# Optimization experiments

Measured on AMD Instinct MI355X. Metric: run time of the kernel, lower is better.

The kernel has to match this reference:

```python
import jax, jax.numpy as jnp
import numpy as np

T, D, N = 131072, 512, 8


def setup_inputs() -> dict:
    key = jax.random.key(0)
    k1, k2, k3, k4 = jax.random.split(key, 4)
    x = jax.random.normal(k1, (T, D), dtype=jnp.float32)
    branch_idx = jax.random.randint(k2, (T,), 0, N, dtype=jnp.int32)
    # module inits weight to identity and bias to zero; use random values
    # (scaled like a trained projection) for a meaningful correctness test
    weight = jax.random.normal(k3, (N, D, D), dtype=jnp.float32) * (1.0 / np.sqrt(D))
    bias = jax.random.normal(k4, (N, D), dtype=jnp.float32) * 0.02
    return {"x": x, "branch_idx": branch_idx, "weight": weight, "bias": bias}


def reference(x, branch_idx, weight, bias):
    # Math: out[t] = x[t] @ weight[branch_idx[t]] + bias[branch_idx[t]]
    # Instead of materializing the gathered (T, D, D) weight tensor (as the
    # naive torch code does), run one dense GEMM per branch and select the
    # rows belonging to that branch. Same result, far less HBM traffic.
    num_branches = weight.shape[0]
    out = jnp.take(bias, branch_idx, axis=0)  # (T, D) gathered bias
    for n in range(num_branches):  # small fixed loop over branches
        mask = (branch_idx == n)[:, None]  # (T, 1)
        out = out + jnp.where(mask, x @ weight[n], jnp.zeros((), x.dtype))
    return out
```

## Files before the change

### kernel.cpp

```cpp
#include <hip/hip_runtime.h>
#include <hip/hip_bf16.h>
#include <stdint.h>

#define T_TOK 131072
#define DIM   512
#define NBR   8
#define BM    64
#define BK    32
#define NKT   (DIM / BK)
#define GT    512
#define MT    288

typedef __attribute__((ext_vector_type(8))) __bf16 bf16x8;
typedef __attribute__((ext_vector_type(4))) float  f32x4;

__device__ __forceinline__ unsigned short f2bf(float f) {
  union { float f; unsigned int u; } v; v.f = f;
  unsigned int r = v.u + 0x7fffu + ((v.u >> 16) & 1u);
  return (unsigned short)(r >> 16);
}


__global__ void k_init(int* counts) {
  if (threadIdx.x < NBR) counts[threadIdx.x] = 0;
}

__global__ __launch_bounds__(512) void k_bhist(const int* __restrict__ bidx,
                                               int* __restrict__ counts) {
  __shared__ int h[NBR];
  if (threadIdx.x < NBR) h[threadIdx.x] = 0;
  __syncthreads();
  int t = blockIdx.x * 512 + threadIdx.x;
  atomicAdd(&h[bidx[t]], 1);
  __syncthreads();
  if (threadIdx.x < NBR) atomicAdd(&counts[threadIdx.x], h[threadIdx.x]);
}

__global__ void k_off(const int* __restrict__ counts, int* __restrict__ offsets,
                      int* __restrict__ cursors) {
  if (threadIdx.x == 0) {
    int s = 0;
    for (int n = 0; n < NBR; ++n) { offsets[n] = s; cursors[n] = s; s += counts[n]; }
  }
}

__global__ __launch_bounds__(512) void k_scatter(const int* __restrict__ bidx,
                                                 int* __restrict__ cursors,
                                                 int* __restrict__ perm) {
  __shared__ int h[NBR], base[NBR];
  if (threadIdx.x < NBR) h[threadIdx.x] = 0;
  __syncthreads();
  int t = blockIdx.x * 512 + threadIdx.x;
  int b = bidx[t];
  int rank = atomicAdd(&h[b], 1);
  __syncthreads();
  if (threadIdx.x < NBR)
    base[threadIdx.x] = atomicAdd(&cursors[threadIdx.x], h[threadIdx.x]);
  __syncthreads();
  perm[base[b] + rank] = t;
}

__global__ __launch_bounds__(256) void k_wtrans(const float* __restrict__ W,
                                                unsigned short* __restrict__ Wt) {
  __shared__ float tile[BK][129];
  int blk = blockIdx.x;
  int b  = blk >> 6;
  int kt = (blk >> 2) & 15;
  int cb = blk & 3;
  int t = threadIdx.x;
  #pragma unroll
  for (int i = 0; i < 4; ++i) {
    int idx4 = i * 256 + t;
    int kr = idx4 >> 5;
    int c4 = idx4 & 31;
    const float* src = W + (((size_t)b * DIM + (size_t)(kt * BK + kr)) * DIM + cb * 128 + c4 * 4);
    float4 v = *(const float4*)src;
    tile[kr][c4 * 4 + 0] = v.x;
    tile[kr][c4 * 4 + 1] = v.y;
    tile[kr][c4 * 4 + 2] = v.z;
    tile[kr][c4 * 4 + 3] = v.w;
  }
  __syncthreads();
  int c  = t >> 1;
  int kh = t & 1;
  unsigned int p[8];
  #pragma unroll
  for (int i = 0; i < 8; ++i) {
    unsigned short lo = f2bf(tile[kh * 16 + i * 2 + 0][c]);
    unsigned short hi = f2bf(tile[kh * 16 + i * 2 + 1][c]);
    p[i] = (unsigned int)lo | ((unsigned int)hi << 16);
  }
  size_t obase = (((size_t)b * 16 + kt) * DIM + (size_t)(cb * 128 + c)) * BK + kh * 16;
  uint4 q0; q0.x = p[0]; q0.y = p[1]; q0.z = p[2]; q0.w = p[3];
  uint4 q1; q1.x = p[4]; q1.y = p[5]; q1.z = p[6]; q1.w = p[7];
  *(uint4*)&Wt[obase]     = q0;
  *(uint4*)&Wt[obase + 8] = q1;
}

__global__ __launch_bounds__(GT, 4)
void k_gemm(const float* __restrict__ x, const float* __restrict__ bias,
            const unsigned short* __restrict__ Wt,
            const int* __restrict__ counts, const int* __restrict__ offsets,
            const int* __restrict__ perm, float* __restrict__ out) {
  __shared__ __align__(16) unsigned short As[2][BM * 40];
  __shared__ int rowIdx[BM];

  const int tid = threadIdx.x;
  const int l = tid & 63;
  const int w = tid >> 6;

  const int b  = blockIdx.x / MT;
  const int lt = blockIdx.x % MT;
  const int cnt = counts[b];
  const int row0 = lt * BM;
  if (row0 >= cnt) return;
  const int gstart = offsets[b];
  const int vrows = min(BM, cnt - row0);

  if (tid < BM) {
    int r = row0 + tid; if (r >= cnt) r = cnt - 1;
    rowIdx[tid] = perm[gstart + r];
  }
  __syncthreads();

  const int arow = tid >> 3;
  const int kq = tid & 7;
  const float* aptr = x + (size_t)rowIdx[arow] * DIM + kq * 4;

  const unsigned short* wtile = Wt + (size_t)b * (NKT * BK * DIM);
  int bBase[4];
  #pragma unroll
  for (int cf = 0; cf < 4; ++cf)
    bBase[cf] = (w * 64 + cf * 16 + (l & 15)) * BK + (l >> 4) * 8;

  const int a_off = (l & 15) * 40 + (l >> 4) * 8;

  f32x4 acc[4][4];
  #pragma unroll
  for (int rf = 0; rf < 4; ++rf)
    #pragma unroll
    for (int cf = 0; cf < 4; ++cf) acc[rf][cf] = (f32x4){0.f, 0.f, 0.f, 0.f};

  {
    float4 av0 = *(const float4*)aptr;
    ushort4 a4;
    a4.x = f2bf(av0.x); a4.y = f2bf(av0.y); a4.z = f2bf(av0.z); a4.w = f2bf(av0.w);
    *(ushort4*)&As[0][arow * 40 + kq * 4] = a4;
  }
  float4 av1 = *(const float4*)(aptr + BK);
  bf16x8 bq[4];
  #pragma unroll
  for (int cf = 0; cf < 4; ++cf) bq[cf] = *(const bf16x8*)(wtile + bBase[cf]);
  __syncthreads();

  #pragma unroll
  for (int kt = 0; kt < NKT; ++kt) {
    const int cur = kt & 1;
    bf16x8 bq2[4];
    float4 av2;
    if (kt + 1 < NKT) {
      const unsigned short* wtk = wtile + (kt + 1) * (BK * DIM);
      #pragma unroll
      for (int cf = 0; cf < 4; ++cf) bq2[cf] = *(const bf16x8*)(wtk + bBase[cf]);
    }
    if (kt + 2 < NKT)
      av2 = *(const float4*)(aptr + (kt + 2) * BK);

    const unsigned short* asrc = &As[cur][0];
    #pragma unroll
    for (int rf = 0; rf < 4; ++rf) {
      bf16x8 af = *(const bf16x8*)&asrc[rf * 640 + a_off];
      #pragma unroll
      for (int cf = 0; cf < 4; ++cf)
        acc[rf][cf] = __builtin_amdgcn_mfma_f32_16x16x32_bf16(af, bq[cf], acc[rf][cf], 0, 0, 0);
    }

    if (kt + 1 < NKT) {
      ushort4 a4;
      a4.x = f2bf(av1.x); a4.y = f2bf(av1.y); a4.z = f2bf(av1.z); a4.w = f2bf(av1.w);
      *(ushort4*)&As[cur ^ 1][arow * 40 + kq * 4] = a4;
      #pragma unroll
      for (int cf = 0; cf < 4; ++cf) bq[cf] = bq2[cf];
    }
    if (kt + 2 < NKT) av1 = av2;
    __syncthreads();
  }

  float bv[4];
  #pragma unroll
  for (int cf = 0; cf < 4; ++cf) bv[cf] = bias[b * DIM + w * 64 + cf * 16 + (l & 15)];
  const int rb = (l >> 4) * 4;
  #pragma unroll
  for (int rf = 0; rf < 4; ++rf) {
    #pragma unroll
    for (int j = 0; j < 4; ++j) {
      int r = rf * 16 + rb + j;
      if (r < vrows) {
        float* op = out + (size_t)rowIdx[r] * DIM + w * 64 + (l & 15);
        #pragma unroll
        for (int cf = 0; cf < 4; ++cf) op[cf * 16] = acc[rf][cf][j] + bv[cf];
      }
    }
  }
}

extern "C" void kernel_launch(void* const* d_in, const int* in_sizes, int n_in,
                              void* d_out, int out_size, void* d_ws, size_t ws_size,
                              hipStream_t stream) {
  const float* x    = (const float*)d_in[0];
  const int*   bidx = (const int*)d_in[1];
  const float* W    = (const float*)d_in[2];
  const float* bias = (const float*)d_in[3];
  float* out = (float*)d_out;

  char* ws = (char*)d_ws;
  int* counts  = (int*)(ws + 0);
  int* cursors = (int*)(ws + 64);
  int* offsets = (int*)(ws + 128);
  int* perm    = (int*)(ws + 256);
  unsigned short* Wt = (unsigned short*)(ws + (1u << 20));

  k_init<<<1, 64, 0, stream>>>(counts);
  k_bhist<<<T_TOK / 512, 512, 0, stream>>>(bidx, counts);
  k_off<<<1, 64, 0, stream>>>(counts, offsets, cursors);
  k_scatter<<<T_TOK / 512, 512, 0, stream>>>(bidx, cursors, perm);
  k_wtrans<<<512, 256, 0, stream>>>(W, Wt);
  k_gemm<<<NBR * MT, GT, 0, stream>>>(x, bias, Wt, counts, offsets, perm, out);
}
```

Baseline: 206.1 us.

## Stage full A row-tile in LDS once and drop per-k-step barriers

The GEMM kernel now converts the block's entire 64x512 activation tile to bf16 into LDS up front (64 KB, in an MFMA-fragment-ordered layout) and then runs the K loop with no __syncthreads. Before, it double-buffered 32-wide K slices with a barrier each step. This removes the per-iteration barriers and gives conflict-free contiguous fragment reads. In exchange, LDS per block grows from about 10 KB to about 64 KB, which limits occupancy to two blocks per CU, and the x loads are no longer overlapped with MFMA work.

```diff
diff --git a/kernel.cpp b/kernel.cpp
--- a/kernel.cpp
+++ b/kernel.cpp
@@ -13,6 +13,7 @@
 
 typedef __attribute__((ext_vector_type(8))) __bf16 bf16x8;
 typedef __attribute__((ext_vector_type(4))) float  f32x4;
+typedef unsigned short ushort_t;
 
 __device__ __forceinline__ unsigned short f2bf(float f) {
   union { float f; unsigned int u; } v; v.f = f;
@@ -61,7 +62,7 @@
 }
 
 __global__ __launch_bounds__(256) void k_wtrans(const float* __restrict__ W,
-                                                unsigned short* __restrict__ Wt) {
+                                                ushort_t* __restrict__ Wt) {
   __shared__ float tile[BK][129];
   int blk = blockIdx.x;
   int b  = blk >> 6;
@@ -99,10 +100,10 @@
 
 __global__ __launch_bounds__(GT, 4)
 void k_gemm(const float* __restrict__ x, const float* __restrict__ bias,
-            const unsigned short* __restrict__ Wt,
+            const ushort_t* __restrict__ Wt,
             const int* __restrict__ counts, const int* __restrict__ offsets,
             const int* __restrict__ perm, float* __restrict__ out) {
-  __shared__ __align__(16) unsigned short As[2][BM * 40];
+  __shared__ __align__(16) ushort_t As[NKT * 4 * 64 * 8];
   __shared__ int rowIdx[BM];
 
   const int tid = threadIdx.x;
@@ -126,64 +127,60 @@
   const int arow = tid >> 3;
   const int kq = tid & 7;
   const float* aptr = x + (size_t)rowIdx[arow] * DIM + kq * 4;
-
-  const unsigned short* wtile = Wt + (size_t)b * (NKT * BK * DIM);
+  const int wbase = (((arow >> 4) * 64) + (kq >> 1) * 16 + (arow & 15)) * 8 + (kq & 1) * 4;
+
+  {
+    float4 xa = *(const float4*)aptr;
+    float4 xb = *(const float4*)(aptr + BK);
+    #pragma unroll
+    for (int i = 0; i < NKT; ++i) {
+      float4 xn;
+      if (i + 2 < NKT) xn = *(const float4*)(aptr + (i + 2) * BK);
+      ushort4 a4;
+      a4.x = f2bf(xa.x); a4.y = f2bf(xa.y); a4.z = f2bf(xa.z); a4.w = f2bf(xa.w);
+      *(ushort4*)&As[i * 2048 + wbase] = a4;
+      xa = xb; xb = xn;
+    }
+  }
+  __syncthreads();
+
+  const ushort_t* wtile = Wt + (size_t)b * (NKT * BK * DIM);
   int bBase[4];
   #pragma unroll
   for (int cf = 0; cf < 4; ++cf)
     bBase[cf] = (w * 64 + cf * 16 + (l & 15)) * BK + (l >> 4) * 8;
 
-  const int a_off = (l & 15) * 40 + (l >> 4) * 8;
-
   f32x4 acc[4][4];
   #pragma unroll
   for (int rf = 0; rf < 4; ++rf)
     #pragma unroll
     for (int cf = 0; cf < 4; ++cf) acc[rf][cf] = (f32x4){0.f, 0.f, 0.f, 0.f};
 
-  {
-    float4 av0 = *(const float4*)aptr;
-    ushort4 a4;
-    a4.x = f2bf(av0.x); a4.y = f2bf(av0.y); a4.z = f2bf(av0.z); a4.w = f2bf(av0.w);
-    *(ushort4*)&As[0][arow * 40 + kq * 4] = a4;
-  }
-  float4 av1 = *(const float4*)(aptr + BK);
   bf16x8 bq[4];
   #pragma unroll
   for (int cf = 0; cf < 4; ++cf) bq[cf] = *(const bf16x8*)(wtile + bBase[cf]);
-  __syncthreads();
 
   #pragma unroll
   for (int kt = 0; kt < NKT; ++kt) {
-    const int cur = kt & 1;
-    bf16x8 bq2[4];
-    float4 av2;
+    bf16x8 bqn[4];
     if (kt + 1 < NKT) {
-      const unsigned short* wtk = wtile + (kt + 1) * (BK * DIM);
+      const ushort_t* wtk = wtile + (kt + 1) * (BK * DIM);
       #pragma unroll
-      for (int cf = 0; cf < 4; ++cf) bq2[cf] = *(const bf16x8*)(wtk + bBase[cf]);
-    }
-    if (kt + 2 < NKT)
-      av2 = *(const float4*)(aptr + (kt + 2) * BK);
-
-    const unsigned short* asrc = &As[cur][0];
-    #pragma unroll
-    for (int rf = 0; rf < 4; ++rf) {
-      bf16x8 af = *(const bf16x8*)&asrc[rf * 640 + a_off];
+      for (int cf = 0; cf < 4; ++cf) bqn[cf] = *(const bf16x8*)(wtk + bBase[cf]);
+    }
+    bf16x8 af[4];
+    #pragma unroll
+    for (int rf = 0; rf < 4; ++rf)
+      af[rf] = *(const bf16x8*)&As[(kt * 4 + rf) * 512 + l * 8];
+    #pragma unroll
+    for (int cf = 0; cf < 4; ++cf)
       #pragma unroll
-      for (int cf = 0; cf < 4; ++cf)
-        acc[rf][cf] = __builtin_amdgcn_mfma_f32_16x16x32_bf16(af, bq[cf], acc[rf][cf], 0, 0, 0);
-    }
-
+      for (int rf = 0; rf < 4; ++rf)
+        acc[rf][cf] = __builtin_amdgcn_mfma_f32_16x16x32_bf16(af[rf], bq[cf], acc[rf][cf], 0, 0, 0);
     if (kt + 1 < NKT) {
-      ushort4 a4;
-      a4.x = f2bf(av1.x); a4.y = f2bf(av1.y); a4.z = f2bf(av1.z); a4.w = f2bf(av1.w);
-      *(ushort4*)&As[cur ^ 1][arow * 40 + kq * 4] = a4;
       #pragma unroll
-      for (int cf = 0; cf < 4; ++cf) bq[cf] = bq2[cf];
-    }
-    if (kt + 2 < NKT) av1 = av2;
-    __syncthreads();
+      for (int cf = 0; cf < 4; ++cf) bq[cf] = bqn[cf];
+    }
   }
 
   float bv[4];
@@ -218,7 +215,7 @@
   int* cursors = (int*)(ws + 64);
   int* offsets = (int*)(ws + 128);
   int* perm    = (int*)(ws + 256);
-  unsigned short* Wt = (unsigned short*)(ws + (1u << 20));
+  ushort_t* Wt = (ushort_t*)(ws + (1u << 20));
 
   k_init<<<1, 64, 0, stream>>>(counts);
   k_bhist<<<T_TOK / 512, 512, 0, stream>>>(bidx, counts);
```

Result: no change. 205.8 us (-0.1%).
